# Kernel tuning notes

Measured on AMD Instinct MI355X. Metric: run time of the kernel, lower is better.

## Reference

```python
import jax, jax.numpy as jnp
import numpy as np

N_EMBED = 1024
N_HEAD = 16
EPS = 1.1920929e-07  # torch.finfo(float32).eps, nn.RMSNorm default eps=None


def rmsnorm(x, w):
    var = jnp.mean(x * x, axis=-1, keepdims=True)
    return x * jax.lax.rsqrt(var + EPS) * w


def setup_inputs() -> dict:
    key = jax.random.key(0)
    ks = jax.random.split(key, 12)
    d = N_EMBED
    s = lambda fan_in: 1.0 / np.sqrt(fan_in)
    inp = {
        "x": jax.random.normal(ks[0], (2, 2048, d), jnp.float32),
        "w_attn": jax.random.uniform(ks[1], (d, 3 * d), jnp.float32, -s(d), s(d)),
        "b_attn": jax.random.uniform(ks[2], (3 * d,), jnp.float32, -s(d), s(d)),
        "w_proj": jax.random.uniform(ks[3], (d, d), jnp.float32, -s(d), s(d)),
        "b_proj": jax.random.uniform(ks[4], (d,), jnp.float32, -s(d), s(d)),
        "w_fc1": jax.random.uniform(ks[5], (d, 4 * d), jnp.float32, -s(d), s(d)),
        "b_fc1": jax.random.uniform(ks[6], (4 * d,), jnp.float32, -s(d), s(d)),
        "w_fc2": jax.random.uniform(ks[7], (4 * d, d), jnp.float32, -s(4 * d), s(4 * d)),
        "b_fc2": jax.random.uniform(ks[8], (d,), jnp.float32, -s(4 * d), s(4 * d)),
        "g_norm1": jnp.ones((d,), jnp.float32),
        "g_norm2": jnp.ones((d,), jnp.float32),
    }
    return inp


def reference(x, w_attn, b_attn, w_proj, b_proj, w_fc1, b_fc1, w_fc2, b_fc2, g_norm1, g_norm2):
    B, T, d = x.shape
    H = N_HEAD
    hd = d // H

    # --- attention branch ---
    h = rmsnorm(x, g_norm1)
    qkv = h @ w_attn + b_attn  # [B,T,3d]
    q, k, v = jnp.split(qkv, 3, axis=-1)
    q = q.reshape(B, T, H, hd).transpose(0, 2, 1, 3)  # [B,H,T,hd]
    k = k.reshape(B, T, H, hd).transpose(0, 2, 1, 3)
    v = v.reshape(B, T, H, hd).transpose(0, 2, 1, 3)
    qk = jnp.einsum('bhqd,bhkd->bhqk', q, k)  # NOTE: no logit scaling (as in source)
    mask = jnp.tril(jnp.ones((T, T), bool))
    qk = jnp.where(mask, qk, -jnp.inf)
    # source scales softmax OUTPUT by n_embed**-0.5 (faithful quirk)
    attn = jax.nn.softmax(qk, axis=-1) * (d ** -0.5)
    o = jnp.einsum('bhqk,bhkd->bhqd', attn, v)
    o = o.transpose(0, 2, 1, 3).reshape(B, T, d)
    x = x + (o @ w_proj + b_proj)

    # --- MLP branch ---
    h = rmsnorm(x, g_norm2)
    h = jax.nn.gelu(h @ w_fc1 + b_fc1, approximate=False)
    x = x + (h @ w_fc2 + b_fc2)
    return x
```

## Files before the change

### kernel.cpp

```cpp
#include <hip/hip_runtime.h>
#include <hip/hip_bf16.h>


typedef __hip_bfloat16 bf16;
typedef __attribute__((ext_vector_type(8))) short short8;
typedef __attribute__((ext_vector_type(4))) float floatx4;

__device__ __forceinline__ float bits2f(unsigned short u) {
  union { unsigned int i; float f; } c; c.i = ((unsigned int)u) << 16; return c.f;
}
__device__ __forceinline__ unsigned short f2bits(float f) {
  bf16 b = __float2bfloat16(f);
  union { bf16 b; unsigned short u; } c; c.b = b; return c.u;
}

__device__ __forceinline__ void gld_lds16(const unsigned short* g, unsigned short* l) {
  __builtin_amdgcn_global_load_lds(
      (const __attribute__((address_space(1))) void*)g,
      (__attribute__((address_space(3))) void*)l, 16, 0, 0);
}

__global__ __launch_bounds__(256) void rmsnorm_r12(const float* __restrict__ x,
                                                   const float* __restrict__ g,
                                                   unsigned short* __restrict__ out)
{
  const int row = blockIdx.x, tid = threadIdx.x;
  const size_t rb = (size_t)row * 1024;
  float4 xv = *(const float4*)(x + rb + tid * 4);
  float v[4] = {xv.x, xv.y, xv.z, xv.w};
  float s = v[0]*v[0] + v[1]*v[1] + v[2]*v[2] + v[3]*v[3];
  #pragma unroll
  for (int off = 32; off > 0; off >>= 1) s += __shfl_down(s, off, 64);
  __shared__ float part[4];
  if ((tid & 63) == 0) part[tid >> 6] = s;
  __syncthreads();
  const float tot = part[0] + part[1] + part[2] + part[3];
  const float sc = rsqrtf(tot * (1.0f / 1024.0f) + 1.1920929e-07f);
  float4 gv = *(const float4*)(g + tid * 4);
  ushort4 o4 = { f2bits(v[0] * sc * gv.x), f2bits(v[1] * sc * gv.y),
                 f2bits(v[2] * sc * gv.z), f2bits(v[3] * sc * gv.w) };
  *(ushort4*)(out + rb + tid * 4) = o4;
}

__global__ __launch_bounds__(256) void wprep_r12(const float* __restrict__ in,
                                                 unsigned short* __restrict__ out,
                                                 int K, int N)
{
  __shared__ unsigned short tile[32][33];
  const int tid = threadIdx.x;
  const int k0 = blockIdx.y * 32, n0 = blockIdx.x * 32;
  const int tr = tid >> 3, tc4 = (tid & 7) * 4;
  float4 v = *(const float4*)(in + (size_t)(k0 + tr) * N + n0 + tc4);
  tile[tr][tc4 + 0] = f2bits(v.x);
  tile[tr][tc4 + 1] = f2bits(v.y);
  tile[tr][tc4 + 2] = f2bits(v.z);
  tile[tr][tc4 + 3] = f2bits(v.w);
  __syncthreads();
  ushort4 o = { tile[tc4 + 0][tr], tile[tc4 + 1][tr],
                tile[tc4 + 2][tr], tile[tc4 + 3][tr] };
  *(ushort4*)(out + (size_t)(n0 + tr) * K + k0 + tc4) = o;
}

template<int EPI>
__global__ __launch_bounds__(256) void gemm_r12(
    const unsigned short* __restrict__ A,
    const unsigned short* __restrict__ BT,
    const float* __restrict__ bias,
    const float* __restrict__ resid,
    void* __restrict__ Cout,
    int M, int N, int K, int Klen)
{
  __shared__ __align__(16) unsigned short As[2][128 * 32];
  __shared__ __align__(16) unsigned short Bs[2][128 * 32];
  const int tid = threadIdx.x;
  const int lane = tid & 63;
  const int wv = tid >> 6;
  const int m0 = blockIdx.y * 128, n0 = blockIdx.x * 128;
  const int wm = (wv >> 1) * 64, wn = (wv & 1) * 64;
  const int kbase = blockIdx.z * Klen;

  const int s0 = tid, s1 = tid + 256;
  const int r0 = s0 >> 2, kq0 = (s0 & 3) ^ ((r0 >> 1) & 3);
  const int r1 = s1 >> 2, kq1 = (s1 & 3) ^ ((r1 >> 1) & 3);
  const unsigned short* Ab = A  + (size_t)m0 * K;
  const unsigned short* Bb = BT + (size_t)n0 * K;
  const size_t ga0 = (size_t)r0 * K + kq0 * 8 + kbase;
  const size_t ga1 = (size_t)r1 * K + kq1 * 8 + kbase;

  floatx4 acc[4][4];
  #pragma unroll
  for (int i = 0; i < 4; ++i)
    #pragma unroll
    for (int j = 0; j < 4; ++j)
      acc[i][j] = (floatx4){0.f, 0.f, 0.f, 0.f};

  int aoff[4], boff[4];
  #pragma unroll
  for (int i = 0; i < 4; ++i) {
    int ra = wm + i * 16 + (lane & 15);
    aoff[i] = (ra * 4 + ((lane >> 4) ^ ((ra >> 1) & 3))) * 8;
    int rb = wn + i * 16 + (lane & 15);
    boff[i] = (rb * 4 + ((lane >> 4) ^ ((rb >> 1) & 3))) * 8;
  }

  gld_lds16(Ab + ga0, As[0] + s0 * 8);
  gld_lds16(Ab + ga1, As[0] + s1 * 8);
  gld_lds16(Bb + ga0, Bs[0] + s0 * 8);
  gld_lds16(Bb + ga1, Bs[0] + s1 * 8);
  __syncthreads();

  const int nsteps = Klen >> 5;
  for (int t = 0; t < nsteps; ++t) {
    const int cur = t & 1;
    if (t + 1 < nsteps) {
      const size_t ko = (size_t)(t + 1) * 32;
      gld_lds16(Ab + ga0 + ko, As[cur ^ 1] + s0 * 8);
      gld_lds16(Ab + ga1 + ko, As[cur ^ 1] + s1 * 8);
      gld_lds16(Bb + ga0 + ko, Bs[cur ^ 1] + s0 * 8);
      gld_lds16(Bb + ga1 + ko, Bs[cur ^ 1] + s1 * 8);
    }

    short8 af[4], bfr[4];
    #pragma unroll
    for (int i = 0; i < 4; ++i) {
      af[i]  = *(const short8*)(As[cur] + aoff[i]);
      bfr[i] = *(const short8*)(Bs[cur] + boff[i]);
    }
    #pragma unroll
    for (int i = 0; i < 4; ++i)
      #pragma unroll
      for (int j = 0; j < 4; ++j)
        acc[i][j] = __builtin_amdgcn_mfma_f32_16x16x32_bf16(af[i], bfr[j], acc[i][j], 0, 0, 0);

    __syncthreads();
  }

  float* Cp32 = (float*)Cout;
  if constexpr (EPI == 4) Cp32 += (size_t)blockIdx.z * ((size_t)M * N);

  #pragma unroll
  for (int i = 0; i < 4; ++i) {
    #pragma unroll
    for (int j = 0; j < 4; ++j) {
      const int rbase = m0 + wm + i * 16 + (lane >> 4) * 4;
      const int c = n0 + wn + j * 16 + (lane & 15);
      float bia = 0.0f;
      if constexpr (EPI != 4) bia = bias[c];
      #pragma unroll
      for (int r = 0; r < 4; ++r) {
        float v = acc[i][j][r] + bia;
        const size_t idx = (size_t)(rbase + r) * N + c;
        if constexpr (EPI == 0) {
          ((unsigned short*)Cout)[idx] = f2bits(v);
        } else if constexpr (EPI == 1) {
          ((float*)Cout)[idx] = v + resid[idx];
        } else if constexpr (EPI == 2) {
          v = 0.5f * v * (1.0f + erff(v * 0.70710678118654752f));
          ((unsigned short*)Cout)[idx] = f2bits(v);
        } else if constexpr (EPI == 3) {
          ((float*)Cout)[idx] = v + resid[idx];
        } else {
          Cp32[idx] = v;
        }
      }
    }
  }
}

__global__ __launch_bounds__(256) void red2_r12(const float* __restrict__ P,
                                                const float* __restrict__ resid,
                                                const float* __restrict__ bias,
                                                float* __restrict__ out)
{
  const size_t i = ((size_t)blockIdx.x * 256 + threadIdx.x) * 4;
  const int col = (int)(i & 1023);
  float4 p0 = *(const float4*)(P + i);
  float4 p1 = *(const float4*)(P + ((size_t)4096 * 1024) + i);
  float4 xr = *(const float4*)(resid + i);
  float4 b  = *(const float4*)(bias + col);
  float4 o  = { p0.x + p1.x + xr.x + b.x, p0.y + p1.y + xr.y + b.y,
                p0.z + p1.z + xr.z + b.z, p0.w + p1.w + xr.w + b.w };
  *(float4*)(out + i) = o;
}

__global__ __launch_bounds__(512) void attn_r12(const unsigned short* __restrict__ qkv,
                                                unsigned short* __restrict__ o)
{
  __shared__ __align__(16) unsigned short Ks[2][64 * 64];
  __shared__ __align__(16) unsigned short VT[2][64 * 72];
  __shared__ __align__(16) unsigned short Ps[128 * 72];
  __shared__ __align__(16) float stat_s[128];

  const int tid = threadIdx.x, lane = tid & 63, wv = tid >> 6;
  const int quad = lane >> 4, l15 = lane & 15;
  const int bid = blockIdx.x;
  const int qt = (bid < 256) ? (15 - (bid >> 5)) : ((bid - 256) >> 5);
  const int bh = bid & 31;
  const int b = bh >> 4, h = bh & 15;
  const size_t base = (size_t)b * 2048 * 3072;
  const int qcol = h * 64, kcol = 1024 + h * 64, vcol = 2048 + h * 64;
  const int q0 = qt * 128;
  const int nkt = 2 * qt + 2;

  const int sr = tid >> 3, scp = tid & 7, sc = scp ^ (sr & 7);
  const unsigned short* kgp = qkv + base + (size_t)sr * 3072 + kcol + sc * 8;
  const int vp = tid & 31, vdc = tid >> 5;
  const unsigned short* vgp = qkv + base + (size_t)(2 * vp) * 3072 + vcol + vdc * 4;

  unsigned short* Qstage = &Ks[0][0];
  #pragma unroll
  for (int p = 0; p < 2; ++p) {
    int s = tid + 512 * p;
    int r = s >> 3, cp = s & 7, c = cp ^ (r & 7);
    gld_lds16(qkv + base + (size_t)(q0 + r) * 3072 + qcol + c * 8, Qstage + s * 8);
  }
  uint2 v0a = *(const uint2*)vgp;
  uint2 v0b = *(const uint2*)(vgp + 3072);
  __syncthreads();

  short8 qa[2];
  #pragma unroll
  for (int ks = 0; ks < 2; ++ks) {
    int ra = wv * 16 + l15;
    int cp = (ks * 4 + quad) ^ (ra & 7);
    qa[ks] = *(const short8*)(Qstage + (ra * 8 + cp) * 8);
  }
  __syncthreads();

  gld_lds16(kgp, Ks[0] + tid * 8);
  {
    unsigned short* dst = VT[0] + (size_t)(vdc * 4) * 72 + 2 * vp;
    *(unsigned int*)(dst + 0 * 72) = (v0a.x & 0xffffu) | (v0b.x << 16);
    *(unsigned int*)(dst + 1 * 72) = (v0a.x >> 16)     | (v0b.x & 0xffff0000u);
    *(unsigned int*)(dst + 2 * 72) = (v0a.y & 0xffffu) | (v0b.y << 16);
    *(unsigned int*)(dst + 3 * 72) = (v0a.y >> 16)     | (v0b.y & 0xffff0000u);
  }
  __syncthreads();

  floatx4 oacc[4];
  #pragma unroll
  for (int dt = 0; dt < 4; ++dt) oacc[dt] = (floatx4){0.f, 0.f, 0.f, 0.f};
  float m_i[4], l_i[4];
  #pragma unroll
  for (int r = 0; r < 4; ++r) { m_i[r] = -3.0e38f; l_i[r] = 0.0f; }

  for (int kt = 0; kt < nkt; ++kt) {
    const int cur = kt & 1;
    const bool pf = (kt + 1 < nkt);
    uint2 u0, u1;
    if (pf) {
      const size_t koff = (size_t)(kt + 1) * 64 * 3072;
      gld_lds16(kgp + koff, Ks[cur ^ 1] + tid * 8);
      u0 = *(const uint2*)(vgp + koff);
      u1 = *(const uint2*)(vgp + koff + 3072);
    }

    short8 kb[4][2];
    #pragma unroll
    for (int j = 0; j < 4; ++j)
      #pragma unroll
      for (int ks = 0; ks < 2; ++ks) {
        int rb = j * 16 + l15;
        int cp = (ks * 4 + quad) ^ (rb & 7);
        kb[j][ks] = *(const short8*)(Ks[cur] + (rb * 8 + cp) * 8);
      }
    floatx4 s_[4];
    #pragma unroll
    for (int j = 0; j < 4; ++j) s_[j] = (floatx4){0.f, 0.f, 0.f, 0.f};
    #pragma unroll
    for (int j = 0; j < 4; ++j)
      #pragma unroll
      for (int ks = 0; ks < 2; ++ks)
        s_[j] = __builtin_amdgcn_mfma_f32_16x16x32_bf16(qa[ks], kb[j][ks], s_[j], 0, 0, 0);

    const int k0 = kt * 64;
    const int rowmin = q0 + wv * 16;
    const int rowb = rowmin + quad * 4;
    if (k0 + 63 > rowmin) {
      #pragma unroll
      for (int j = 0; j < 4; ++j) {
        const int col = k0 + j * 16 + l15;
        #pragma unroll
        for (int r = 0; r < 4; ++r)
          if (col > rowb + r) s_[j][r] = -3.0e38f;
      }
    }
    float fm[4], al[4], rs[4];
    #pragma unroll
    for (int r = 0; r < 4; ++r)
      fm[r] = fmaxf(fmaxf(s_[0][r], s_[1][r]), fmaxf(s_[2][r], s_[3][r]));
    #pragma unroll
    for (int msk = 1; msk < 16; msk <<= 1)
      #pragma unroll
      for (int r = 0; r < 4; ++r)
        fm[r] = fmaxf(fm[r], __shfl_xor(fm[r], msk, 64));
    #pragma unroll
    for (int r = 0; r < 4; ++r) {
      const float mn = fmaxf(m_i[r], fm[r]);
      al[r] = __expf(m_i[r] - mn);
      m_i[r] = mn;
    }
    #pragma unroll
    for (int j = 0; j < 4; ++j)
      #pragma unroll
      for (int r = 0; r < 4; ++r)
        s_[j][r] = __expf(s_[j][r] - m_i[r]);
    #pragma unroll
    for (int r = 0; r < 4; ++r)
      rs[r] = (s_[0][r] + s_[1][r]) + (s_[2][r] + s_[3][r]);
    #pragma unroll
    for (int msk = 1; msk < 16; msk <<= 1)
      #pragma unroll
      for (int r = 0; r < 4; ++r)
        rs[r] += __shfl_xor(rs[r], msk, 64);
    #pragma unroll
    for (int r = 0; r < 4; ++r)
      l_i[r] = l_i[r] * al[r] + rs[r];
    if (l15 == 0) {
      float4 a4 = { al[0], al[1], al[2], al[3] };
      *(float4*)(stat_s + wv * 16 + quad * 4) = a4;
    }
    #pragma unroll
    for (int j = 0; j < 4; ++j)
      #pragma unroll
      for (int r = 0; r < 4; ++r)
        Ps[(size_t)(wv * 16 + quad * 4 + r) * 72 + j * 16 + l15] = f2bits(s_[j][r]);

    const float alq = stat_s[wv * 16 + l15];
    #pragma unroll
    for (int dt = 0; dt < 4; ++dt)
      #pragma unroll
      for (int r = 0; r < 4; ++r)
        oacc[dt][r] *= alq;

    short8 va[4][2], pb[2];
    #pragma unroll
    for (int dt = 0; dt < 4; ++dt)
      #pragma unroll
      for (int ks = 0; ks < 2; ++ks)
        va[dt][ks] = *(const short8*)(VT[cur] + (size_t)(dt * 16 + l15) * 72 + ks * 32 + quad * 8);
    #pragma unroll
    for (int ks = 0; ks < 2; ++ks)
      pb[ks] = *(const short8*)(Ps + (size_t)(wv * 16 + l15) * 72 + ks * 32 + quad * 8);
    #pragma unroll
    for (int dt = 0; dt < 4; ++dt)
      #pragma unroll
      for (int ks = 0; ks < 2; ++ks)
        oacc[dt] = __builtin_amdgcn_mfma_f32_16x16x32_bf16(va[dt][ks], pb[ks], oacc[dt], 0, 0, 0);

    if (pf) {
      unsigned short* dst = VT[cur ^ 1] + (size_t)(vdc * 4) * 72 + 2 * vp;
      *(unsigned int*)(dst + 0 * 72) = (u0.x & 0xffffu) | (u1.x << 16);
      *(unsigned int*)(dst + 1 * 72) = (u0.x >> 16)     | (u1.x & 0xffff0000u);
      *(unsigned int*)(dst + 2 * 72) = (u0.y & 0xffffu) | (u1.y << 16);
      *(unsigned int*)(dst + 3 * 72) = (u0.y >> 16)     | (u1.y & 0xffff0000u);
    }
    __syncthreads();
  }

  if (l15 == 0) {
    float4 l4 = { l_i[0], l_i[1], l_i[2], l_i[3] };
    *(float4*)(stat_s + wv * 16 + quad * 4) = l4;
  }
  const float linv = 0.03125f / stat_s[wv * 16 + l15];
  const size_t row = (size_t)b * 2048 + q0 + wv * 16 + l15;
  #pragma unroll
  for (int dt = 0; dt < 4; ++dt) {
    const int col = h * 64 + dt * 16 + quad * 4;
    ushort4 o4 = { f2bits(oacc[dt][0] * linv), f2bits(oacc[dt][1] * linv),
                   f2bits(oacc[dt][2] * linv), f2bits(oacc[dt][3] * linv) };
    *(ushort4*)(o + row * 1024 + col) = o4;
  }
}

extern "C" void kernel_launch(void* const* d_in, const int* in_sizes, int n_in,
                              void* d_out, int out_size, void* d_ws, size_t ws_size,
                              hipStream_t stream)
{
  (void)in_sizes; (void)n_in; (void)out_size; (void)ws_size;
  const float* x      = (const float*)d_in[0];
  const float* w_attn = (const float*)d_in[1];
  const float* b_attn = (const float*)d_in[2];
  const float* w_proj = (const float*)d_in[3];
  const float* b_proj = (const float*)d_in[4];
  const float* w_fc1  = (const float*)d_in[5];
  const float* b_fc1  = (const float*)d_in[6];
  const float* w_fc2  = (const float*)d_in[7];
  const float* b_fc2  = (const float*)d_in[8];
  const float* g1     = (const float*)d_in[9];
  const float* g2     = (const float*)d_in[10];
  float* out = (float*)d_out;

  char* ws = (char*)d_ws;
  unsigned short* h   = (unsigned short*)(ws);
  unsigned short* qkv = (unsigned short*)(ws + ((size_t)8  << 20));
  unsigned short* ov  = (unsigned short*)(ws);
  float*          x1  = (float*)         (ws + ((size_t)32 << 20));
  unsigned short* h2  = (unsigned short*)(ws + ((size_t)8  << 20));
  unsigned short* h3  = (unsigned short*)(ws + ((size_t)48 << 20));
  unsigned short* WT  = (unsigned short*)(ws + ((size_t)80 << 20));
  float*          P   = (float*)(ws);

  const int M = 4096;

  rmsnorm_r12<<<M, 256, 0, stream>>>(x, g1, h);
  wprep_r12<<<dim3(3072 / 32, 1024 / 32), 256, 0, stream>>>(w_attn, WT, 1024, 3072);
  gemm_r12<0><<<dim3(3072 / 128, M / 128), 256, 0, stream>>>(h, WT, b_attn, nullptr, qkv, M, 3072, 1024, 1024);
  attn_r12<<<dim3(512), 512, 0, stream>>>(qkv, ov);
  wprep_r12<<<dim3(1024 / 32, 1024 / 32), 256, 0, stream>>>(w_proj, WT, 1024, 1024);
  gemm_r12<1><<<dim3(1024 / 128, M / 128), 256, 0, stream>>>(ov, WT, b_proj, x, x1, M, 1024, 1024, 1024);
  rmsnorm_r12<<<M, 256, 0, stream>>>(x1, g2, h2);
  wprep_r12<<<dim3(4096 / 32, 1024 / 32), 256, 0, stream>>>(w_fc1, WT, 1024, 4096);
  gemm_r12<2><<<dim3(4096 / 128, M / 128), 256, 0, stream>>>(h2, WT, b_fc1, nullptr, h3, M, 4096, 1024, 1024);
  wprep_r12<<<dim3(1024 / 32, 4096 / 32), 256, 0, stream>>>(w_fc2, WT, 4096, 1024);
  gemm_r12<4><<<dim3(1024 / 128, M / 128, 2), 256, 0, stream>>>(h3, WT, nullptr, nullptr, P, M, 1024, 4096, 2048);
  red2_r12<<<4096, 256, 0, stream>>>(P, x1, b_fc2, out);
}
```

Before: 394.8 us.

## Split long causal attention tiles across two blocks and merge partials

Measured after the change: 407.9 us. 1.03x slower.

```diff
diff --git a/kernel.cpp b/kernel.cpp
--- a/kernel.cpp
+++ b/kernel.cpp
@@ -20,7 +20,7 @@
       (__attribute__((address_space(3))) void*)l, 16, 0, 0);
 }
 
-__global__ __launch_bounds__(256) void rmsnorm_r12(const float* __restrict__ x,
+__global__ __launch_bounds__(256) void rmsnorm_r13(const float* __restrict__ x,
                                                    const float* __restrict__ g,
                                                    unsigned short* __restrict__ out)
 {
@@ -42,7 +42,7 @@
   *(ushort4*)(out + rb + tid * 4) = o4;
 }
 
-__global__ __launch_bounds__(256) void wprep_r12(const float* __restrict__ in,
+__global__ __launch_bounds__(256) void wprep_r13(const float* __restrict__ in,
                                                  unsigned short* __restrict__ out,
                                                  int K, int N)
 {
@@ -62,7 +62,7 @@
 }
 
 template<int EPI>
-__global__ __launch_bounds__(256) void gemm_r12(
+__global__ __launch_bounds__(256) void gemm_r13(
     const unsigned short* __restrict__ A,
     const unsigned short* __restrict__ BT,
     const float* __restrict__ bias,
@@ -167,7 +167,7 @@
   }
 }
 
-__global__ __launch_bounds__(256) void red2_r12(const float* __restrict__ P,
+__global__ __launch_bounds__(256) void red2_r13(const float* __restrict__ P,
                                                 const float* __restrict__ resid,
                                                 const float* __restrict__ bias,
                                                 float* __restrict__ out)
@@ -183,8 +183,10 @@
   *(float4*)(out + i) = o;
 }
 
-__global__ __launch_bounds__(512) void attn_r12(const unsigned short* __restrict__ qkv,
-                                                unsigned short* __restrict__ o)
+__global__ __launch_bounds__(512) void attn_r13(const unsigned short* __restrict__ qkv,
+                                                unsigned short* __restrict__ o,
+                                                float* __restrict__ Opart,
+                                                float* __restrict__ MLpart)
 {
   __shared__ __align__(16) unsigned short Ks[2][64 * 64];
   __shared__ __align__(16) unsigned short VT[2][64 * 72];
@@ -194,13 +196,23 @@
   const int tid = threadIdx.x, lane = tid & 63, wv = tid >> 6;
   const int quad = lane >> 4, l15 = lane & 15;
   const int bid = blockIdx.x;
-  const int qt = (bid < 256) ? (15 - (bid >> 5)) : ((bid - 256) >> 5);
-  const int bh = bid & 31;
+  const int t = bid & 255, batch = bid >> 8;
+  const int p = t >> 5, bh = t & 31;
+  int qt, kt0, ktN, pi = -1;
+  if (batch < 2) {
+    qt = 15 - p;
+    kt0 = batch ? (qt + 1) : 0;
+    ktN = batch ? (2 * qt + 2) : (qt + 1);
+    pi = (p * 32 + bh) * 2 + batch;
+  } else {
+    qt = p;
+    kt0 = 0;
+    ktN = 2 * qt + 2;
+  }
   const int b = bh >> 4, h = bh & 15;
   const size_t base = (size_t)b * 2048 * 3072;
   const int qcol = h * 64, kcol = 1024 + h * 64, vcol = 2048 + h * 64;
   const int q0 = qt * 128;
-  const int nkt = 2 * qt + 2;
 
   const int sr = tid >> 3, scp = tid & 7, sc = scp ^ (sr & 7);
   const unsigned short* kgp = qkv + base + (size_t)sr * 3072 + kcol + sc * 8;
@@ -209,13 +221,14 @@
 
   unsigned short* Qstage = &Ks[0][0];
   #pragma unroll
-  for (int p = 0; p < 2; ++p) {
-    int s = tid + 512 * p;
+  for (int pp = 0; pp < 2; ++pp) {
+    int s = tid + 512 * pp;
     int r = s >> 3, cp = s & 7, c = cp ^ (r & 7);
     gld_lds16(qkv + base + (size_t)(q0 + r) * 3072 + qcol + c * 8, Qstage + s * 8);
   }
-  uint2 v0a = *(const uint2*)vgp;
-  uint2 v0b = *(const uint2*)(vgp + 3072);
+  const size_t koff0 = (size_t)kt0 * 64 * 3072;
+  uint2 v0a = *(const uint2*)(vgp + koff0);
+  uint2 v0b = *(const uint2*)(vgp + koff0 + 3072);
   __syncthreads();
 
   short8 qa[2];
@@ -227,7 +240,7 @@
   }
   __syncthreads();
 
-  gld_lds16(kgp, Ks[0] + tid * 8);
+  gld_lds16(kgp + koff0, Ks[0] + tid * 8);
   {
     unsigned short* dst = VT[0] + (size_t)(vdc * 4) * 72 + 2 * vp;
     *(unsigned int*)(dst + 0 * 72) = (v0a.x & 0xffffu) | (v0b.x << 16);
@@ -244,9 +257,9 @@
   #pragma unroll
   for (int r = 0; r < 4; ++r) { m_i[r] = -3.0e38f; l_i[r] = 0.0f; }
 
-  for (int kt = 0; kt < nkt; ++kt) {
-    const int cur = kt & 1;
-    const bool pf = (kt + 1 < nkt);
+  for (int kt = kt0; kt < ktN; ++kt) {
+    const int cur = (kt - kt0) & 1;
+    const bool pf = (kt + 1 < ktN);
     uint2 u0, u1;
     if (pf) {
       const size_t koff = (size_t)(kt + 1) * 64 * 3072;
@@ -358,18 +371,68 @@
     __syncthreads();
   }
 
-  if (l15 == 0) {
-    float4 l4 = { l_i[0], l_i[1], l_i[2], l_i[3] };
-    *(float4*)(stat_s + wv * 16 + quad * 4) = l4;
-  }
-  const float linv = 0.03125f / stat_s[wv * 16 + l15];
-  const size_t row = (size_t)b * 2048 + q0 + wv * 16 + l15;
-  #pragma unroll
-  for (int dt = 0; dt < 4; ++dt) {
-    const int col = h * 64 + dt * 16 + quad * 4;
-    ushort4 o4 = { f2bits(oacc[dt][0] * linv), f2bits(oacc[dt][1] * linv),
-                   f2bits(oacc[dt][2] * linv), f2bits(oacc[dt][3] * linv) };
-    *(ushort4*)(o + row * 1024 + col) = o4;
+  if (batch < 2) {
+    float* Ob = Opart + (size_t)pi * (128 * 64);
+    const int q = wv * 16 + l15;
+    #pragma unroll
+    for (int dt = 0; dt < 4; ++dt) {
+      float4 o4 = { oacc[dt][0], oacc[dt][1], oacc[dt][2], oacc[dt][3] };
+      *(float4*)(Ob + q * 64 + dt * 16 + quad * 4) = o4;
+    }
+    if (l15 == 0) {
+      float* Mb = MLpart + (size_t)pi * 256;
+      #pragma unroll
+      for (int r = 0; r < 4; ++r) {
+        Mb[wv * 16 + quad * 4 + r]       = m_i[r];
+        Mb[128 + wv * 16 + quad * 4 + r] = l_i[r];
+      }
+    }
+  } else {
+    if (l15 == 0) {
+      float4 l4 = { l_i[0], l_i[1], l_i[2], l_i[3] };
+      *(float4*)(stat_s + wv * 16 + quad * 4) = l4;
+    }
+    const float linv = 0.03125f / stat_s[wv * 16 + l15];
+    const size_t row = (size_t)b * 2048 + q0 + wv * 16 + l15;
+    #pragma unroll
+    for (int dt = 0; dt < 4; ++dt) {
+      const int col = h * 64 + dt * 16 + quad * 4;
+      ushort4 o4 = { f2bits(oacc[dt][0] * linv), f2bits(oacc[dt][1] * linv),
+                     f2bits(oacc[dt][2] * linv), f2bits(oacc[dt][3] * linv) };
+      *(ushort4*)(o + row * 1024 + col) = o4;
+    }
+  }
+}
+
+__global__ __launch_bounds__(256) void amerge_r13(const float* __restrict__ Opart,
+                                                  const float* __restrict__ MLpart,
+                                                  unsigned short* __restrict__ o)
+{
+  const int p = blockIdx.x, bh = blockIdx.y;
+  const int qt = 15 - p, b = bh >> 4, h = bh & 15;
+  const int pi0 = (p * 32 + bh) * 2;
+  const float* O1 = Opart + (size_t)pi0 * (128 * 64);
+  const float* O2 = O1 + 128 * 64;
+  const float* ML1 = MLpart + (size_t)pi0 * 256;
+  const float* ML2 = ML1 + 256;
+  const int tid = threadIdx.x;
+  const int q = tid >> 1, d0 = (tid & 1) * 32;
+  const float m1 = ML1[q], l1 = ML1[128 + q];
+  const float m2 = ML2[q], l2 = ML2[128 + q];
+  const float m = fmaxf(m1, m2);
+  const float a1 = __expf(m1 - m), a2 = __expf(m2 - m);
+  const float inv = 0.03125f / (l1 * a1 + l2 * a2);
+  const size_t row = (size_t)b * 2048 + qt * 128 + q;
+  unsigned short* ob = o + row * 1024 + h * 64 + d0;
+  #pragma unroll
+  for (int e = 0; e < 8; ++e) {
+    float4 o1 = *(const float4*)(O1 + q * 64 + d0 + e * 4);
+    float4 o2 = *(const float4*)(O2 + q * 64 + d0 + e * 4);
+    ushort4 o4 = { f2bits((o1.x * a1 + o2.x * a2) * inv),
+                   f2bits((o1.y * a1 + o2.y * a2) * inv),
+                   f2bits((o1.z * a1 + o2.z * a2) * inv),
+                   f2bits((o1.w * a1 + o2.w * a2) * inv) };
+    *(ushort4*)(ob + e * 4) = o4;
   }
 }
 
@@ -400,19 +463,22 @@
   unsigned short* h3  = (unsigned short*)(ws + ((size_t)48 << 20));
   unsigned short* WT  = (unsigned short*)(ws + ((size_t)80 << 20));
   float*          P   = (float*)(ws);
+  float*          Op  = (float*)(ws + ((size_t)48 << 20));
+  float*          MLp = (float*)(ws + ((size_t)65 << 20));
 
   const int M = 4096;
 
-  rmsnorm_r12<<<M, 256, 0, stream>>>(x, g1, h);
-  wprep_r12<<<dim3(3072 / 32, 1024 / 32), 256, 0, stream>>>(w_attn, WT, 1024, 3072);
-  gemm_r12<0><<<dim3(3072 / 128, M / 128), 256, 0, stream>>>(h, WT, b_attn, nullptr, qkv, M, 3072, 1024, 1024);
-  attn_r12<<<dim3(512), 512, 0, stream>>>(qkv, ov);
-  wprep_r12<<<dim3(1024 / 32, 1024 / 32), 256, 0, stream>>>(w_proj, WT, 1024, 1024);
-  gemm_r12<1><<<dim3(1024 / 128, M / 128), 256, 0, stream>>>(ov, WT, b_proj, x, x1, M, 1024, 1024, 1024);
-  rmsnorm_r12<<<M, 256, 0, stream>>>(x1, g2, h2);
-  wprep_r12<<<dim3(4096 / 32, 1024 / 32), 256, 0, stream>>>(w_fc1, WT, 1024, 4096);
-  gemm_r12<2><<<dim3(4096 / 128, M / 128), 256, 0, stream>>>(h2, WT, b_fc1, nullptr, h3, M, 4096, 1024, 1024);
-  wprep_r12<<<dim3(1024 / 32, 4096 / 32), 256, 0, stream>>>(w_fc2, WT, 4096, 1024);
-  gemm_r12<4><<<dim3(1024 / 128, M / 128, 2), 256, 0, stream>>>(h3, WT, nullptr, nullptr, P, M, 1024, 4096, 2048);
-  red2_r12<<<4096, 256, 0, stream>>>(P, x1, b_fc2, out);
-}
+  rmsnorm_r13<<<M, 256, 0, stream>>>(x, g1, h);
+  wprep_r13<<<dim3(3072 / 32, 1024 / 32), 256, 0, stream>>>(w_attn, WT, 1024, 3072);
+  gemm_r13<0><<<dim3(3072 / 128, M / 128), 256, 0, stream>>>(h, WT, b_attn, nullptr, qkv, M, 3072, 1024, 1024);
+  attn_r13<<<dim3(768), 512, 0, stream>>>(qkv, ov, Op, MLp);
+  amerge_r13<<<dim3(8, 32), 256, 0, stream>>>(Op, MLp, ov);
+  wprep_r13<<<dim3(1024 / 32, 1024 / 32), 256, 0, stream>>>(w_proj, WT, 1024, 1024);
+  gemm_r13<1><<<dim3(1024 / 128, M / 128), 256, 0, stream>>>(ov, WT, b_proj, x, x1, M, 1024, 1024, 1024);
+  rmsnorm_r13<<<M, 256, 0, stream>>>(x1, g2, h2);
+  wprep_r13<<<dim3(4096 / 32, 1024 / 32), 256, 0, stream>>>(w_fc1, WT, 1024, 4096);
+  gemm_r13<2><<<dim3(4096 / 128, M / 128), 256, 0, stream>>>(h2, WT, b_fc1, nullptr, h3, M, 4096, 1024, 1024);
+  wprep_r13<<<dim3(1024 / 32, 4096 / 32), 256, 0, stream>>>(w_fc2, WT, 4096, 1024);
+  gemm_r13<4><<<dim3(1024 / 128, M / 128, 2), 256, 0, stream>>>(h3, WT, nullptr, nullptr, P, M, 1024, 4096, 2048);
+  red2_r13<<<4096, 256, 0, stream>>>(P, x1, b_fc2, out);
+}
```
